# Optimization experiments

Measured on AMD Instinct MI355X. Metric: run time of the kernel, lower is better.

## Reference

```python
import jax, jax.numpy as jnp
import numpy as np
from jax import lax


def setup_inputs() -> dict:
    key = jax.random.key(0)
    ks = jax.random.split(key, 6)
    B, S, C, HID, H, K = 8, 2048, 768, 768, 12, 9
    return {
        "query": jax.random.normal(ks[0], (B, S, C), jnp.float32),
        "value": jax.random.normal(ks[1], (B, S, C), jnp.float32),
        "hidden_states": jax.random.normal(ks[2], (B, S, HID), jnp.float32),
        "dw_weight": jax.random.normal(ks[3], (HID, 1, K), jnp.float32) * (2.0 / K) ** 0.5,
        "pw_weight": jax.random.normal(ks[4], (C, HID, 1), jnp.float32) * (2.0 / HID) ** 0.5,
        "sep_bias": jnp.zeros((C,), jnp.float32),
        "attn_W": jax.random.normal(ks[5], (H * K, C), jnp.float32) * (1.0 / C) ** 0.5,
        "attn_b": jnp.zeros((H * K,), jnp.float32),
        "num_heads": H,
        "kernel_size": K,
    }


def reference(query, value, hidden_states, dw_weight, pw_weight, sep_bias,
              attn_W, attn_b, num_heads, kernel_size):
    K = kernel_size
    H = num_heads
    B, S, C = value.shape  # all_head_size = C
    D = C // H             # attention_head_size
    HID = hidden_states.shape[-1]
    pad = K // 2

    # --- SeparableConv1d: depthwise (groups=HID) then pointwise 1x1 ---
    x = jnp.transpose(hidden_states, (0, 2, 1))  # [B, HID, S]
    dn = ("NCH", "OIH", "NCH")
    dw = lax.conv_general_dilated(x, dw_weight, window_strides=(1,),
                                  padding=[(pad, pad)], dimension_numbers=dn,
                                  feature_group_count=HID)  # [B, HID, S]
    pw = lax.conv_general_dilated(dw, pw_weight, window_strides=(1,),
                                  padding=[(0, 0)], dimension_numbers=dn)  # [B, C, S]
    ks_out = jnp.transpose(pw, (0, 2, 1)) + sep_bias  # [B, S, C]

    # --- dynamic conv kernel: gated projection + (double) softmax ---
    conv_attn = ks_out * query                                   # [B, S, C]
    filt = conv_attn @ attn_W.T + attn_b                          # [B, S, H*K]
    filt = filt.reshape(B, S, H, K)
    # original code applies softmax twice (once in SDConv, once in LightConv)
    filt = jax.nn.softmax(jax.nn.softmax(filt, axis=-1), axis=-1)

    # --- light conv: unfold value along seq and contract over window ---
    vpad = jnp.pad(value, ((0, 0), (pad, pad), (0, 0)))           # [B, S+K-1, C]
    unf = jnp.stack([vpad[:, k:k + S, :] for k in range(K)], axis=-1)  # [B,S,C,K]
    unf = unf.reshape(B, S, H, D, K)
    out = jnp.einsum("bshdk,bshk->bshd", unf, filt)               # [B,S,H,D]
    return out
```

## Files before the change

### kernel.cpp

```cpp
#include <hip/hip_runtime.h>
#include <hip/hip_bf16.h>
#include <stdint.h>

#define B_   8
#define S_   2048
#define C_   768
#define HID_ 768
#define H_   12
#define KW   9
#define D_   64
#define M_   (B_ * S_)
#define PADW 4
#define HK_  108
#define NPAD 128

typedef __attribute__((ext_vector_type(4))) float  floatx4;
typedef __attribute__((ext_vector_type(8))) __bf16 bf16x8;

#define GLD_LDS16(gptr, lptr)                                                  \
    __builtin_amdgcn_global_load_lds(                                          \
        (__attribute__((address_space(1))) void*)(gptr),                       \
        (__attribute__((address_space(3))) void*)(lptr), 16, 0, 0)

#define BARR() do { __builtin_amdgcn_s_barrier();                              \
                    __builtin_amdgcn_sched_barrier(0); } while (0)
#define LGKM0() do { asm volatile("s_waitcnt lgkmcnt(0)" ::: "memory");        \
                     __builtin_amdgcn_sched_barrier(0); } while (0)

__global__ __launch_bounds__(256) void convert_w_kernel(
    const float* __restrict__ pwW, const float* __restrict__ attnW,
    __hip_bfloat16* __restrict__ pwWb, __hip_bfloat16* __restrict__ attnWb)
{
    int i = blockIdx.x * 256 + threadIdx.x;
    if (i < C_ * HID_) pwWb[i] = __float2bfloat16(pwW[i]);
    if (i < NPAD * HID_) {
        int n = i / HID_;
        float v = (n < HK_) ? attnW[i] : 0.0f;
        attnWb[i] = __float2bfloat16(v);
    }
}

#define TSD 16

__global__ __launch_bounds__(256) void dwconv_kernel(
    const float* __restrict__ hidden, const float* __restrict__ dw_w,
    __hip_bfloat16* __restrict__ dw_out)
{
    int idx  = blockIdx.x * 256 + threadIdx.x;
    int hq   = idx % (HID_ / 4);
    int rest = idx / (HID_ / 4);
    int sc   = rest % (S_ / TSD);
    int b    = rest / (S_ / TSD);
    int h    = hq * 4;
    int s0   = sc * TSD;
    size_t base = (size_t)b * S_ * HID_ + h;

    float w[36];
    const float4* wp = reinterpret_cast<const float4*>(dw_w + (size_t)h * KW);
#pragma unroll
    for (int i = 0; i < 9; ++i) {
        float4 t = wp[i];
        w[4 * i + 0] = t.x; w[4 * i + 1] = t.y;
        w[4 * i + 2] = t.z; w[4 * i + 3] = t.w;
    }

    float4 win[KW];
#pragma unroll
    for (int k = 0; k < 8; ++k) {
        int sp = s0 + k - PADW;
        float4 v = {0.f, 0.f, 0.f, 0.f};
        if ((unsigned)sp < (unsigned)S_)
            v = *reinterpret_cast<const float4*>(&hidden[base + (size_t)sp * HID_]);
        win[k] = v;
    }

#pragma unroll
    for (int i = 0; i < TSD; ++i) {
        int sp = s0 + i + PADW;
        float4 nv = {0.f, 0.f, 0.f, 0.f};
        if ((unsigned)sp < (unsigned)S_)
            nv = *reinterpret_cast<const float4*>(&hidden[base + (size_t)sp * HID_]);
        win[8] = nv;

        float a0 = 0.f, a1 = 0.f, a2 = 0.f, a3 = 0.f;
#pragma unroll
        for (int k = 0; k < KW; ++k) {
            a0 += win[k].x * w[k];
            a1 += win[k].y * w[9 + k];
            a2 += win[k].z * w[18 + k];
            a3 += win[k].w * w[27 + k];
        }
        union { __hip_bfloat16 bv[4]; uint2 u; } o;
        o.bv[0] = __float2bfloat16(a0);
        o.bv[1] = __float2bfloat16(a1);
        o.bv[2] = __float2bfloat16(a2);
        o.bv[3] = __float2bfloat16(a3);
        *reinterpret_cast<uint2*>(&dw_out[base + (size_t)(s0 + i) * HID_]) = o.u;

#pragma unroll
        for (int k = 0; k < 8; ++k) win[k] = win[k + 1];
    }
}

__global__ __launch_bounds__(256, 2) void fused_gemm_kernel(
    const __hip_bfloat16* __restrict__ A,
    const __hip_bfloat16* __restrict__ Bt,
    const __hip_bfloat16* __restrict__ Wt,
    const float* __restrict__ bias,
    const float* __restrict__ query,
    const float* __restrict__ attn_b,
    float* __restrict__ filt)
{
    __shared__ __align__(16) char lds[73728];
    char* Plds = lds + 8192;
    float* LG  = (float*)(lds + 8192 + 32768);

    const int t    = threadIdx.x;
    const int lane = t & 63;
    const int wave = t >> 6;
    const int l16  = lane & 15, lq = lane >> 4;

    const int row0 = (int)blockIdx.x * 32;

    const int sr8     = lane >> 3;
    const int srcslot = (lane & 7) ^ sr8;
    const __hip_bfloat16* aS = A + (size_t)(row0 + wave * 8 + sr8) * HID_ + srcslot * 8;

    floatx4 acc2[2][2];
#pragma unroll
    for (int m = 0; m < 2; ++m)
#pragma unroll
        for (int n = 0; n < 2; ++n) acc2[m][n] = (floatx4){0.f, 0.f, 0.f, 0.f};

    for (int nt = 0; nt < 3; ++nt) {
        const __hip_bfloat16* bS =
            Bt + (size_t)(nt * 256 + wave * 64 + sr8) * HID_ + srcslot * 8;

        floatx4 acc1[2][4];
#pragma unroll
        for (int m = 0; m < 2; ++m)
#pragma unroll
            for (int n = 0; n < 4; ++n) acc1[m][n] = (floatx4){0.f, 0.f, 0.f, 0.f};

#define FSTG(kt, buf) do {                                                     \
        GLD_LDS16(aS + (kt) * 64, lds + (buf) * 4096 + wave * 1024);           \
        _Pragma("unroll")                                                      \
        for (int _i = 0; _i < 8; ++_i)                                         \
            GLD_LDS16(bS + (size_t)_i * 8 * HID_ + (kt) * 64,                  \
                      lds + 8192 + (buf) * 32768 + wave * 8192 + _i * 1024);   \
    } while (0)

        FSTG(0, 0);
#pragma unroll 2
        for (int kt = 0; kt < 12; ++kt) {
            const int cur = kt & 1;
            if (kt < 11) {
                FSTG(kt + 1, cur ^ 1);
                asm volatile("s_waitcnt vmcnt(9)" ::: "memory");
            } else {
                asm volatile("s_waitcnt vmcnt(0)" ::: "memory");
            }
            __builtin_amdgcn_sched_barrier(0);
            BARR();

            const char* ab = lds + cur * 4096;
            const char* bb = lds + 8192 + cur * 32768;
            bf16x8 av[2][2], bv[4][2];
#pragma unroll
            for (int m = 0; m < 2; ++m) {
                const int r = m * 16 + l16;
#pragma unroll
                for (int ks = 0; ks < 2; ++ks)
                    av[m][ks] = *(const bf16x8*)(ab + r * 128 +
                        ((ks * 64 + lq * 16) ^ ((l16 & 7) << 4)));
            }
#pragma unroll
            for (int n = 0; n < 4; ++n) {
                const int r = wave * 64 + n * 16 + l16;
#pragma unroll
                for (int ks = 0; ks < 2; ++ks)
                    bv[n][ks] = *(const bf16x8*)(bb + r * 128 +
                        ((ks * 64 + lq * 16) ^ ((l16 & 7) << 4)));
            }
            __builtin_amdgcn_s_setprio(1);
#pragma unroll
            for (int m = 0; m < 2; ++m)
#pragma unroll
                for (int n = 0; n < 4; ++n)
#pragma unroll
                    for (int ks = 0; ks < 2; ++ks)
                        acc1[m][n] = __builtin_amdgcn_mfma_f32_16x16x32_bf16(
                            av[m][ks], bv[n][ks], acc1[m][n], 0, 0, 0);
            __builtin_amdgcn_s_setprio(0);
            LGKM0();
            BARR();
        }
#undef FSTG

#pragma unroll
        for (int m = 0; m < 2; ++m)
#pragma unroll
            for (int n = 0; n < 4; ++n) {
                const int cl   = wave * 64 + n * 16 + l16;
                const int gcol = nt * 256 + cl;
                const float bvv = bias[gcol];
#pragma unroll
                for (int j = 0; j < 4; ++j) {
                    const int row = m * 16 + lq * 4 + j;
                    float v = (acc1[m][n][j] + bvv) *
                              query[(size_t)(row0 + row) * C_ + gcol];
                    __hip_bfloat16 hb = __float2bfloat16(v);
                    *(uint16_t*)(Plds + row * 512 +
                                 ((cl * 2) ^ ((row & 7) << 4))) =
                        *(uint16_t*)&hb;
                }
            }
        LGKM0();
        BARR();

#pragma unroll
        for (int kk = 0; kk < 8; ++kk) {
            bf16x8 pv[2], wv[2];
#pragma unroll
            for (int m = 0; m < 2; ++m) {
                const int r = m * 16 + l16;
                pv[m] = *(const bf16x8*)(Plds + r * 512 +
                    ((kk * 64 + lq * 16) ^ ((l16 & 7) << 4)));
            }
#pragma unroll
            for (int n = 0; n < 2; ++n) {
                const int wrow = wave * 32 + n * 16 + l16;
                wv[n] = *(const bf16x8*)(Wt + (size_t)wrow * C_ +
                                         nt * 256 + kk * 32 + lq * 8);
            }
#pragma unroll
            for (int m = 0; m < 2; ++m)
#pragma unroll
                for (int n = 0; n < 2; ++n)
                    acc2[m][n] = __builtin_amdgcn_mfma_f32_16x16x32_bf16(
                        pv[m], wv[n], acc2[m][n], 0, 0, 0);
        }
        LGKM0();
        BARR();
    }

#pragma unroll
    for (int m = 0; m < 2; ++m)
#pragma unroll
        for (int n = 0; n < 2; ++n) {
            const int cl = wave * 32 + n * 16 + l16;
#pragma unroll
            for (int j = 0; j < 4; ++j) {
                const int row = m * 16 + lq * 4 + j;
                LG[row * 128 + cl] = acc2[m][n][j];
            }
        }
    LGKM0();
    BARR();

    for (int id = t; id < 32 * H_; id += 256) {
        const int row = id / H_;
        const int h   = id - row * H_;
        float v[KW];
#pragma unroll
        for (int k = 0; k < KW; ++k)
            v[k] = LG[row * 128 + h * KW + k] + attn_b[h * KW + k];
#pragma unroll
        for (int pass = 0; pass < 2; ++pass) {
            float mx = v[0];
#pragma unroll
            for (int k = 1; k < KW; ++k) mx = fmaxf(mx, v[k]);
            float s = 0.f;
#pragma unroll
            for (int k = 0; k < KW; ++k) { v[k] = __expf(v[k] - mx); s += v[k]; }
            float inv = 1.f / s;
#pragma unroll
            for (int k = 0; k < KW; ++k) v[k] *= inv;
        }
        const size_t base = ((size_t)(row0 + row) * H_ + h) * KW;
#pragma unroll
        for (int k = 0; k < KW; ++k) filt[base + k] = v[k];
    }
}

#define TSL 16
#define SCHK 256

__global__ __launch_bounds__(256) void lightconv_kernel(
    const float* __restrict__ value, const float* __restrict__ filt,
    float* __restrict__ out)
{
    __shared__ float fl[SCHK * KW];

    const int tid = threadIdx.x;
    const int blk = blockIdx.x;
    const int nSC = S_ / SCHK;
    const int b   = blk / (H_ * nSC);
    const int rem = blk % (H_ * nSC);
    const int h   = rem / nSC;
    const int sch = rem % nSC;
    const int S0  = sch * SCHK;

    {
        const size_t r0 = ((size_t)b * S_ + S0) * H_ + h;
#pragma unroll
        for (int i = 0; i < 9; ++i) {
            int j  = tid + 256 * i;
            int so = j / KW;
            int k  = j - so * KW;
            fl[j] = filt[(r0 + (size_t)so * H_) * KW + k];
        }
    }
    __syncthreads();

    const int d4 = tid & 15;
    const int sg = tid >> 4;
    const int s0 = S0 + sg * TSL;
    const size_t vbase = (size_t)b * S_ * C_ + h * D_ + d4 * 4;
    const float* flrow = &fl[(sg * TSL) * KW];

    float4 win[KW];
#pragma unroll
    for (int k = 0; k < 8; ++k) {
        int sp = s0 + k - PADW;
        float4 v = {0.f, 0.f, 0.f, 0.f};
        if ((unsigned)sp < (unsigned)S_)
            v = *reinterpret_cast<const float4*>(&value[vbase + (size_t)sp * C_]);
        win[k] = v;
    }

#pragma unroll
    for (int i = 0; i < TSL; ++i) {
        int sp = s0 + i + PADW;
        float4 nv = {0.f, 0.f, 0.f, 0.f};
        if ((unsigned)sp < (unsigned)S_)
            nv = *reinterpret_cast<const float4*>(&value[vbase + (size_t)sp * C_]);
        win[8] = nv;

        float4 acc = {0.f, 0.f, 0.f, 0.f};
#pragma unroll
        for (int k = 0; k < KW; ++k) {
            float f = flrow[i * KW + k];
            acc.x += win[k].x * f;
            acc.y += win[k].y * f;
            acc.z += win[k].z * f;
            acc.w += win[k].w * f;
        }
        *reinterpret_cast<float4*>(&out[vbase + (size_t)(s0 + i) * C_]) = acc;

#pragma unroll
        for (int k = 0; k < 8; ++k) win[k] = win[k + 1];
    }
}

extern "C" void kernel_launch(void* const* d_in, const int* in_sizes, int n_in,
                              void* d_out, int out_size, void* d_ws, size_t ws_size,
                              hipStream_t stream)
{
    const float* query  = (const float*)d_in[0];
    const float* value  = (const float*)d_in[1];
    const float* hidden = (const float*)d_in[2];
    const float* dw_w   = (const float*)d_in[3];
    const float* pw_w   = (const float*)d_in[4];
    const float* sep_b  = (const float*)d_in[5];
    const float* attn_W = (const float*)d_in[6];
    const float* attn_b = (const float*)d_in[7];
    float* out = (float*)d_out;

    char* ws = (char*)d_ws;
    __hip_bfloat16* dwb    = (__hip_bfloat16*)(ws);
    __hip_bfloat16* pwWb   = (__hip_bfloat16*)(ws + 25165824);
    __hip_bfloat16* attnWb = (__hip_bfloat16*)(ws + 26345472);
    float*          filt   = (float*)(ws + 26542080);

    convert_w_kernel<<<(C_ * HID_) / 256, 256, 0, stream>>>(pw_w, attn_W, pwWb, attnWb);

    dwconv_kernel<<<(M_ * (HID_ / 4)) / (256 * TSD), 256, 0, stream>>>(hidden, dw_w, dwb);

    fused_gemm_kernel<<<M_ / 32, 256, 0, stream>>>(
        dwb, pwWb, attnWb, sep_b, query, attn_b, filt);

    lightconv_kernel<<<B_ * H_ * (S_ / SCHK), 256, 0, stream>>>(value, filt, out);
}
```

Baseline: 94.04 us.

## Load GEMM B fragments directly into registers instead of staging through LDS

In the fused GEMM's first stage, the B operand (pointwise weights) is no longer copied into LDS with global_load_lds. Each wave now loads its own B fragments straight from global memory into a double-buffered register set, using inline global_load_dwordx4. Only the A tile still goes through LDS. Since each wave uses distinct B rows, the LDS round trip was pure overhead, so dropping it removes LDS traffic and shrinks the shared allocation. The trade-off is more VGPR pressure and a less coalesced per-lane global access pattern.

```diff
diff --git a/kernel.cpp b/kernel.cpp
--- a/kernel.cpp
+++ b/kernel.cpp
@@ -27,6 +27,14 @@
 #define LGKM0() do { asm volatile("s_waitcnt lgkmcnt(0)" ::: "memory");        \
                      __builtin_amdgcn_sched_barrier(0); } while (0)
 
+static __device__ __forceinline__ bf16x8 gload16(const __hip_bfloat16* p) {
+    floatx4 r;
+    asm volatile("global_load_dwordx4 %0, %1, off" : "=v"(r) : "v"(p) : "memory");
+    union { floatx4 f; bf16x8 b; } u;
+    u.f = r;
+    return u.b;
+}
+
 __global__ __launch_bounds__(256) void convert_w_kernel(
     const float* __restrict__ pwW, const float* __restrict__ attnW,
     __hip_bfloat16* __restrict__ pwWb, __hip_bfloat16* __restrict__ attnWb)
@@ -111,9 +119,9 @@
     const float* __restrict__ attn_b,
     float* __restrict__ filt)
 {
-    __shared__ __align__(16) char lds[73728];
+    __shared__ __align__(16) char lds[40960];
     char* Plds = lds + 8192;
-    float* LG  = (float*)(lds + 8192 + 32768);
+    float* LG  = (float*)(lds + 24576);
 
     const int t    = threadIdx.x;
     const int lane = t & 63;
@@ -132,9 +140,52 @@
 #pragma unroll
         for (int n = 0; n < 2; ++n) acc2[m][n] = (floatx4){0.f, 0.f, 0.f, 0.f};
 
+#define FSTG_A(kt, buf)                                                        \
+    GLD_LDS16(aS + (kt) * 64, lds + (buf) * 4096 + wave * 1024)
+
+#define BPRE(kt, PRE) do {                                                     \
+    _Pragma("unroll") for (int _nf = 0; _nf < 4; ++_nf)                        \
+        _Pragma("unroll") for (int _ks = 0; _ks < 2; ++_ks)                    \
+            PRE[_nf][_ks] = gload16(bp[_nf] + (kt) * 64 + _ks * 32);           \
+} while (0)
+
+#define STEP(kt, CONS, PRE, cbuf, nbuf, last) do {                             \
+    if (!(last)) {                                                             \
+        FSTG_A((kt) + 1, nbuf);                                                \
+        BPRE((kt) + 1, PRE);                                                   \
+        asm volatile("s_waitcnt vmcnt(9)" ::: "memory");                       \
+    } else {                                                                   \
+        asm volatile("s_waitcnt vmcnt(0)" ::: "memory");                       \
+    }                                                                          \
+    __builtin_amdgcn_sched_barrier(0);                                         \
+    __builtin_amdgcn_s_barrier();                                              \
+    {                                                                          \
+        const char* _ab = lds + (cbuf) * 4096;                                 \
+        bf16x8 _av[2][2];                                                      \
+        _Pragma("unroll") for (int _m = 0; _m < 2; ++_m) {                     \
+            const int _r = _m * 16 + l16;                                      \
+            _Pragma("unroll") for (int _ks = 0; _ks < 2; ++_ks)                \
+                _av[_m][_ks] = *(const bf16x8*)(_ab + _r * 128 +               \
+                    ((_ks * 64 + lq * 16) ^ ((l16 & 7) << 4)));                \
+        }                                                                      \
+        __builtin_amdgcn_s_setprio(1);                                         \
+        _Pragma("unroll") for (int _m = 0; _m < 2; ++_m)                       \
+            _Pragma("unroll") for (int _n = 0; _n < 4; ++_n)                   \
+                _Pragma("unroll") for (int _ks = 0; _ks < 2; ++_ks)            \
+                    acc1[_m][_n] = __builtin_amdgcn_mfma_f32_16x16x32_bf16(    \
+                        _av[_m][_ks], CONS[_n][_ks], acc1[_m][_n], 0, 0, 0);   \
+        __builtin_amdgcn_s_setprio(0);                                         \
+    }                                                                          \
+    LGKM0();                                                                   \
+    BARR();                                                                    \
+} while (0)
+
     for (int nt = 0; nt < 3; ++nt) {
-        const __hip_bfloat16* bS =
-            Bt + (size_t)(nt * 256 + wave * 64 + sr8) * HID_ + srcslot * 8;
+        const __hip_bfloat16* bp[4];
+#pragma unroll
+        for (int nf = 0; nf < 4; ++nf)
+            bp[nf] = Bt + (size_t)(nt * 256 + wave * 64 + nf * 16 + l16) * HID_
+                        + lq * 8;
 
         floatx4 acc1[2][4];
 #pragma unroll
@@ -142,60 +193,15 @@
 #pragma unroll
             for (int n = 0; n < 4; ++n) acc1[m][n] = (floatx4){0.f, 0.f, 0.f, 0.f};
 
-#define FSTG(kt, buf) do {                                                     \
-        GLD_LDS16(aS + (kt) * 64, lds + (buf) * 4096 + wave * 1024);           \
-        _Pragma("unroll")                                                      \
-        for (int _i = 0; _i < 8; ++_i)                                         \
-            GLD_LDS16(bS + (size_t)_i * 8 * HID_ + (kt) * 64,                  \
-                      lds + 8192 + (buf) * 32768 + wave * 8192 + _i * 1024);   \
-    } while (0)
-
-        FSTG(0, 0);
-#pragma unroll 2
-        for (int kt = 0; kt < 12; ++kt) {
-            const int cur = kt & 1;
-            if (kt < 11) {
-                FSTG(kt + 1, cur ^ 1);
-                asm volatile("s_waitcnt vmcnt(9)" ::: "memory");
-            } else {
-                asm volatile("s_waitcnt vmcnt(0)" ::: "memory");
-            }
-            __builtin_amdgcn_sched_barrier(0);
-            BARR();
-
-            const char* ab = lds + cur * 4096;
-            const char* bb = lds + 8192 + cur * 32768;
-            bf16x8 av[2][2], bv[4][2];
-#pragma unroll
-            for (int m = 0; m < 2; ++m) {
-                const int r = m * 16 + l16;
-#pragma unroll
-                for (int ks = 0; ks < 2; ++ks)
-                    av[m][ks] = *(const bf16x8*)(ab + r * 128 +
-                        ((ks * 64 + lq * 16) ^ ((l16 & 7) << 4)));
-            }
-#pragma unroll
-            for (int n = 0; n < 4; ++n) {
-                const int r = wave * 64 + n * 16 + l16;
-#pragma unroll
-                for (int ks = 0; ks < 2; ++ks)
-                    bv[n][ks] = *(const bf16x8*)(bb + r * 128 +
-                        ((ks * 64 + lq * 16) ^ ((l16 & 7) << 4)));
-            }
-            __builtin_amdgcn_s_setprio(1);
-#pragma unroll
-            for (int m = 0; m < 2; ++m)
-#pragma unroll
-                for (int n = 0; n < 4; ++n)
-#pragma unroll
-                    for (int ks = 0; ks < 2; ++ks)
-                        acc1[m][n] = __builtin_amdgcn_mfma_f32_16x16x32_bf16(
-                            av[m][ks], bv[n][ks], acc1[m][n], 0, 0, 0);
-            __builtin_amdgcn_s_setprio(0);
-            LGKM0();
-            BARR();
-        }
-#undef FSTG
+        bf16x8 bregA[4][2], bregB[4][2];
+
+        FSTG_A(0, 0);
+        BPRE(0, bregA);
+
+        for (int kp = 0; kp < 6; ++kp) {
+            STEP(2 * kp,     bregA, bregB, 0, 1, false);
+            STEP(2 * kp + 1, bregB, bregA, 1, 0, (kp == 5));
+        }
 
 #pragma unroll
         for (int m = 0; m < 2; ++m)
@@ -243,6 +249,9 @@
         LGKM0();
         BARR();
     }
+#undef FSTG_A
+#undef BPRE
+#undef STEP
 
 #pragma unroll
     for (int m = 0; m < 2; ++m)
```

Measured after the change: 147.1 us. 1.56x slower.
